# Kernel optimization log

Hardware: AMD Instinct MI355X
Metric: run time of the kernel (lower is better)

The kernel has to match this reference:

```python
import jax, jax.numpy as jnp
import numpy as np

B, T = 32, 64            # batch, max caption length
E = 14                   # encoded image grid
ENC_D, DEC_D, ATT_D = 2048, 512, 512
PATCH, CH = 32, 3
FLAT = PATCH * PATCH * CH   # 3072
EMB = 256
PAD = PATCH // 2 + PATCH // 4  # 24
IMG = 512


def setup_inputs() -> dict:
    key = jax.random.key(0)
    ks = jax.random.split(key, 20)
    w = lambda k, shp: (0.02 * jax.random.normal(k, shp)).astype(jnp.float32)
    z = lambda *shp: jnp.zeros(shp, jnp.float32)
    lengths = jnp.concatenate(
        [jnp.array([[T]], jnp.int32),
         jax.random.randint(ks[4], (B - 1, 1), 1, T + 1, dtype=jnp.int32)], axis=0)
    return dict(
        encoder_out=jax.random.normal(ks[0], (B, E, E, ENC_D), jnp.float32),
        imgs=jax.random.normal(ks[1], (B, CH, IMG, IMG), jnp.float32),
        sequence=jax.random.randint(ks[2], (B, T, 2), 0, IMG - PATCH, dtype=jnp.int32),
        sequence_offset=jax.random.normal(ks[3], (B, T, 2), jnp.float32),
        caption_lengths=lengths,
        W_pe=w(ks[5], (EMB, FLAT)), b_pe=z(EMB),
        W_enc_att=w(ks[6], (ATT_D, ENC_D)), b_enc_att=z(ATT_D),
        W_dec_att=w(ks[7], (ATT_D, DEC_D)), b_dec_att=z(ATT_D),
        w_full=w(ks[8], (ATT_D,)), b_full=jnp.zeros((), jnp.float32),
        W_init_h=w(ks[9], (DEC_D, ENC_D + EMB)), b_init_h=z(DEC_D),
        W_init_c=w(ks[10], (DEC_D, ENC_D + EMB)), b_init_c=z(DEC_D),
        W_fb=w(ks[11], (ENC_D, DEC_D)), b_fb=z(ENC_D),
        W_ih=w(ks[12], (4 * DEC_D, ENC_D + EMB)), b_ih=z(4 * DEC_D),
        W_hh=w(ks[13], (4 * DEC_D, DEC_D)), b_hh=z(4 * DEC_D),
        W_fc=w(ks[14], (2, DEC_D)), b_fc=z(2),
        W_stop=w(ks[15], (1, DEC_D)), b_stop=z(1),
    )


def _extract_patches(imgs, seq):
    # imgs: [B,C,H,W] int keypoints seq: [B,T,2] (x,y); deterministic shift=0
    padded = jnp.pad(imgs, ((0, 0), (0, 0), (PAD, PAD), (PAD, PAD)))
    def one(img, kp):
        return jax.lax.dynamic_slice(img, (0, kp[1], kp[0]), (CH, PATCH, PATCH))
    return jax.vmap(lambda img, kps: jax.vmap(lambda kp: one(img, kp))(kps))(padded, seq)


def reference(encoder_out, imgs, sequence, sequence_offset, caption_lengths,
              W_pe, b_pe, W_enc_att, b_enc_att, W_dec_att, b_dec_att, w_full, b_full,
              W_init_h, b_init_h, W_init_c, b_init_c, W_fb, b_fb,
              W_ih, b_ih, W_hh, b_hh, W_fc, b_fc, W_stop, b_stop):
    lengths = caption_lengths[:, 0]
    sort_ind = jnp.argsort(-lengths)            # descending, like torch sort
    lengths = lengths[sort_ind]
    enc = encoder_out[sort_ind].reshape(B, -1, ENC_D)   # [B,P,ENC_D]
    imgs_s = imgs[sort_ind]
    seq_s = sequence[sort_ind]
    seq_off_s = sequence_offset[sort_ind]

    # patch embedding (dropout is identity in eval mode)
    patches = _extract_patches(imgs_s, seq_s).reshape(B, T, FLAT)
    emb = patches @ W_pe.T + b_pe               # [B,T,EMB]

    # init hidden state
    init_in = jnp.concatenate([enc.mean(axis=1), emb[:, 0, :]], axis=1)
    h = init_in @ W_init_h.T + b_init_h
    c = init_in @ W_init_c.T + b_init_c

    att1 = enc @ W_enc_att.T + b_enc_att        # [B,P,A] (loop-invariant)

    def step(carry, xs):
        h, c = carry
        emb_t, t = xs
        att2 = h @ W_dec_att.T + b_dec_att                       # [B,A]
        scores = jnp.einsum('bpa,a->bp', jax.nn.relu(att1 + att2[:, None, :]), w_full) + b_full
        alpha = jax.nn.softmax(scores, axis=1)                   # [B,P]
        awe = jnp.einsum('bpd,bp->bd', enc, alpha)               # [B,ENC_D]
        gate = jax.nn.sigmoid(h @ W_fb.T + b_fb)
        x = jnp.concatenate([gate * awe, emb_t], axis=1)
        gates = x @ W_ih.T + b_ih + h @ W_hh.T + b_hh
        i, f, g, o = jnp.split(gates, 4, axis=1)
        c_new = jax.nn.sigmoid(f) * c + jax.nn.sigmoid(i) * jnp.tanh(g)
        h_new = jax.nn.sigmoid(o) * jnp.tanh(c_new)
        mask = (t < lengths)[:, None]
        preds = jnp.where(mask, h_new @ W_fc.T + b_fc, 0.0)
        preds_stop = jnp.where(mask, jax.nn.sigmoid(h_new @ W_stop.T + b_stop), 0.0)
        alpha_m = jnp.where(mask, alpha, 0.0)
        h = jnp.where(mask, h_new, h)
        c = jnp.where(mask, c_new, c)
        return (h, c), (preds, preds_stop, alpha_m)

    (_, _), (P, PS, AL) = jax.lax.scan(step, (h, c), (emb.transpose(1, 0, 2), jnp.arange(T)))
    predictions = P.transpose(1, 0, 2)          # [B,T,2]
    predictions_stop = PS.transpose(1, 0, 2)    # [B,T,1]
    alphas = AL.transpose(1, 0, 2)              # [B,T,P]
    return predictions, predictions_stop, seq_off_s, lengths, alphas, sort_ind
```

## Files before the change

kernel.cpp:

```cpp
#include <hip/hip_runtime.h>

#define Bn 32
#define Tn 64
#define Pn 196
#define ENCD 2048
#define DECD 512
#define XDIM 2304

typedef unsigned short u16;
typedef __attribute__((ext_vector_type(8))) short bf16x8;
typedef __attribute__((ext_vector_type(4))) float f32x4;

#define MF(a,b,c) __builtin_amdgcn_mfma_f32_16x16x32_bf16(a,b,c,0,0,0)

static __device__ __forceinline__ u16 f2bf(float f){
  unsigned int u = __float_as_uint(f);
  unsigned int r = u + 0x7FFFu + ((u >> 16) & 1u);
  return (u16)(r >> 16);
}
static __device__ __forceinline__ float bf2f(u16 u){
  return __uint_as_float(((unsigned int)u) << 16);
}

#define O_PRED   0
#define O_STOP   4096
#define O_SEQOFF 6144
#define O_LEN    10240
#define O_ALPHA  10272
#define O_SORT   411680

#define WS_SORT    0
#define WS_LEN     32
#define WS_C       64
#define WS_PA      16448
#define WS_SCP     163904
#define WS_ENCM    215104
#define WS_EMB0    280640
#define WS_BCOMB   288832
#define US_H0      800000
#define US_H1      816384
#define US_XA      832768
#define US_EMBBF   898304
#define US_ATT1T   1422592
#define US_ENC     4830464
#define US_WAP     17675520
#define US_WIHE    20067584
#define US_WIH2    20591872
#define US_GEMB    24786176
#define US_PATCH   20591872
#define US_WPEB    26883328
#define US_WEA     27931904

__global__ void k_prep(const int* __restrict__ caplen, int* __restrict__ ws_sort,
                       int* __restrict__ ws_len, float* __restrict__ out){
  __shared__ int len[32];
  int i = threadIdx.x;
  if (i < 32) len[i] = caplen[i];
  __syncthreads();
  if (i < 32){
    int li = len[i], r = 0;
    for (int j = 0; j < 32; j++){
      int lj = len[j];
      r += (lj > li) || (lj == li && j < i);
    }
    ws_sort[r] = i;
    ws_len[r]  = li;
    out[O_LEN + r]  = (float)li;
    out[O_SORT + r] = (float)i;
  }
}

__global__ __launch_bounds__(256) void k_stageA(const float* __restrict__ enc,
    const float* __restrict__ imgs, const int* __restrict__ seq,
    const float* __restrict__ W_pe, const float* __restrict__ Wea,
    const float* __restrict__ seqoff, const int* __restrict__ srt,
    u16* __restrict__ encbf, float* __restrict__ encm, u16* __restrict__ patches,
    u16* __restrict__ wpeb, u16* __restrict__ wead, float* __restrict__ out){
  int blk = blockIdx.x, tid = threadIdx.x;
  if (blk < 6272){
    int m = blk;
    int b = m / 196, p = m - b*196;
    const float* src = enc + ((size_t)srt[b]*196 + p)*ENCD;
    u16* d = encbf + (size_t)m*ENCD;
    int i = tid*8;
    float4 v0 = *(const float4*)(src + i);
    float4 v1 = *(const float4*)(src + i + 4);
    bf16x8 s;
    s[0]=(short)f2bf(v0.x); s[1]=(short)f2bf(v0.y); s[2]=(short)f2bf(v0.z); s[3]=(short)f2bf(v0.w);
    s[4]=(short)f2bf(v1.x); s[5]=(short)f2bf(v1.y); s[6]=(short)f2bf(v1.z); s[7]=(short)f2bf(v1.w);
    *(bf16x8*)(d + i) = s;
  } else if (blk < 6528){
    int r = blk - 6272;
    int b = r >> 3, dc = r & 7;
    int d = dc*256 + tid;
    const float* ep = enc + ((size_t)srt[b]*196)*ENCD + d;
    float s = 0.f;
    #pragma unroll 4
    for (int p = 0; p < Pn; p++) s += ep[(size_t)p*ENCD];
    encm[b*ENCD + d] = s * (1.f/196.f);
  } else if (blk < 8576){
    int r = blk - 6528;
    int b = r>>6, t = r&63;
    int sb = srt[b];
    int x0 = seq[(sb*64+t)*2 + 0], y0 = seq[(sb*64+t)*2 + 1];
    const float* img = imgs + (size_t)sb*3*512*512;
    u16* dst = patches + (size_t)(b*64+t)*3072;
    for (int idx = tid; idx < 3072; idx += 256){
      int c = idx>>10, rem = idx&1023, i = rem>>5, j = rem&31;
      int yy = y0 + i - 24, xx = x0 + j - 24;
      float v = 0.f;
      if ((unsigned)yy < 512u && (unsigned)xx < 512u) v = img[((size_t)c*512 + yy)*512 + xx];
      dst[idx] = f2bf(v);
    }
  } else if (blk < 9344){
    int i = ((blk - 8576)*256 + tid)*4;
    float4 v = *(const float4*)(W_pe + i);
    wpeb[i+0] = f2bf(v.x); wpeb[i+1] = f2bf(v.y);
    wpeb[i+2] = f2bf(v.z); wpeb[i+3] = f2bf(v.w);
  } else if (blk < 9856){
    int r = blk - 9344;
    for (int i = tid; i < 2048; i += 256)
      wead[(size_t)r*2048 + i] = f2bf(Wea[(size_t)r*2048 + i]);
  } else {
    int idx = (blk - 9856)*256 + tid;
    int b = idx >> 7, r = idx & 127;
    out[O_SEQOFF + idx] = seqoff[srt[b]*128 + r];
  }
}

__global__ __launch_bounds__(256) void k_stageB(const u16* __restrict__ patches,
    const u16* __restrict__ wpeb, const float* __restrict__ b_pe,
    const u16* __restrict__ encbf, const u16* __restrict__ wead,
    const float* __restrict__ bea,
    u16* __restrict__ embbf, float* __restrict__ emb0, u16* __restrict__ att1T){
  __shared__ u16 A[64*138];
  int blk = blockIdx.x, tid = threadIdx.x;
  int wv = tid>>6, lane = tid&63, lr = lane&15, lh = lane>>4;
  if (blk < 128){
    int mb = blk >> 2, nb = blk & 3;
    int m0 = mb*64;
    f32x4 acc[4];
    #pragma unroll
    for (int mt = 0; mt < 4; mt++) acc[mt] = (f32x4){0,0,0,0};
    for (int kc = 0; kc < 24; kc++){
      __syncthreads();
      {
        int row = tid>>2, seg = tid&3;
        const u16* src = patches + (size_t)(m0 + row)*3072 + kc*128 + seg*32;
        #pragma unroll
        for (int i = 0; i < 4; i++)
          *(bf16x8*)&A[row*138 + seg*32 + i*8] = *(const bf16x8*)(src + i*8);
      }
      __syncthreads();
      #pragma unroll
      for (int ki = 0; ki < 4; ki++){
        bf16x8 bv = *(const bf16x8*)&wpeb[(size_t)(nb*64 + wv*16 + lr)*3072 + kc*128 + ki*32 + lh*8];
        #pragma unroll
        for (int mt = 0; mt < 4; mt++){
          bf16x8 av = *(const bf16x8*)&A[(mt*16 + lr)*138 + ki*32 + lh*8];
          acc[mt] = MF(av, bv, acc[mt]);
        }
      }
    }
    int n = nb*64 + wv*16 + lr;
    float bias = b_pe[n];
    #pragma unroll
    for (int mt = 0; mt < 4; mt++){
      #pragma unroll
      for (int r = 0; r < 4; r++){
        int t = mt*16 + lh*4 + r;
        float val = acc[mt][r] + bias;
        embbf[(size_t)(m0 + t)*256 + n] = f2bf(val);
        if (t == 0) emb0[mb*256 + n] = val;
      }
    }
  } else {
    int ab = blk - 128;
    int mb = ab >> 2, nb = ab & 3;
    int m0 = mb*64;
    f32x4 acc[4][2];
    #pragma unroll
    for (int mt = 0; mt < 4; mt++){ acc[mt][0] = (f32x4){0,0,0,0}; acc[mt][1] = (f32x4){0,0,0,0}; }
    for (int kc = 0; kc < 16; kc++){
      __syncthreads();
      {
        int row = tid>>2, seg = tid&3;
        const u16* src = encbf + (size_t)(m0 + row)*2048 + kc*128 + seg*32;
        #pragma unroll
        for (int i = 0; i < 4; i++)
          *(bf16x8*)&A[row*138 + seg*32 + i*8] = *(const bf16x8*)(src + i*8);
      }
      __syncthreads();
      #pragma unroll
      for (int ki = 0; ki < 4; ki++){
        bf16x8 av[4];
        #pragma unroll
        for (int mt = 0; mt < 4; mt++)
          av[mt] = *(const bf16x8*)&A[(mt*16 + lr)*138 + ki*32 + lh*8];
        #pragma unroll
        for (int nt = 0; nt < 2; nt++){
          const u16* wp = wead + (size_t)(nb*128 + wv*32 + nt*16 + lr)*2048 + kc*128 + ki*32 + lh*8;
          bf16x8 bv = *(const bf16x8*)wp;
          #pragma unroll
          for (int mt = 0; mt < 4; mt++) acc[mt][nt] = MF(av[mt], bv, acc[mt][nt]);
        }
      }
    }
    #pragma unroll
    for (int nt = 0; nt < 2; nt++){
      int n = nb*128 + wv*32 + nt*16 + lr;
      float bias = bea[n];
      #pragma unroll
      for (int mt = 0; mt < 4; mt++){
        #pragma unroll
        for (int r = 0; r < 4; r++){
          int m = m0 + mt*16 + lh*4 + r;
          int bb = m / 196, pp = m - bb*196;
          att1T[((size_t)bb*512 + n)*208 + pp] = f2bf(acc[mt][nt][r] + bias);
        }
      }
    }
  }
}

__global__ __launch_bounds__(256) void k_stageC(const float* __restrict__ Wih,
    const float* __restrict__ Whh, const float* __restrict__ Wdec,
    const float* __restrict__ Wfb, const float* __restrict__ Wfc,
    const float* __restrict__ Wstop, const float* __restrict__ bih,
    const float* __restrict__ bhh,
    const float* __restrict__ encm, const float* __restrict__ emb0,
    const float* __restrict__ Wh, const float* __restrict__ Wc,
    u16* __restrict__ WIH2, u16* __restrict__ WIHE, u16* __restrict__ WAP,
    float* __restrict__ bcomb, float* __restrict__ part){
  int blk = blockIdx.x, tid = threadIdx.x;
  if (blk < 2048){
    int r = blk, jp = (r & 511)*4 + (r >> 9);
    for (int i = tid; i < 2304; i += 256){
      u16 v = f2bf(Wih[(size_t)r*2304 + i]);
      if (i < 2048) WIH2[(size_t)jp*2048 + i] = v;
      else          WIHE[(size_t)jp*256 + (i - 2048)] = v;
    }
  } else if (blk < 6720){
    int j = blk - 2048;
    const float* src;
    if (j < 512)        src = Wdec + (size_t)j*512;
    else if (j < 2560)  src = Wfb + (size_t)(j-512)*512;
    else if (j < 4608)  src = Whh + (size_t)(j-2560)*512;
    else if (j == 4608) src = Wfc;
    else if (j == 4609) src = Wfc + 512;
    else if (j == 4610) src = Wstop;
    else src = 0;
    for (int i = tid; i < 512; i += 256)
      WAP[(size_t)j*512 + i] = src ? f2bf(src[i]) : (u16)0;
  } else if (blk < 6728){
    int jp = (blk - 6720)*256 + tid;
    int r = (jp & 3)*512 + (jp >> 2);
    bcomb[jp] = bih[r] + bhh[r];
  } else {
    int ib = blk - 6728;
    int kc = ib >> 4, jb = ib & 15;
    int wv = tid>>6, lane = tid&63, lr = lane&15, lh = lane>>4;
    int j = jb*64 + wv*16 + lr;
    const float* wbase = (j < 512) ? (Wh + (size_t)j*XDIM) : (Wc + (size_t)(j-512)*XDIM);
    f32x4 acc0 = {0,0,0,0}, acc1 = {0,0,0,0};
    #pragma unroll 2
    for (int kk = 0; kk < 576; kk += 32){
      int k = kc*576 + kk + lh*8;
      float4 w0 = *(const float4*)(wbase + k);
      float4 w1 = *(const float4*)(wbase + k + 4);
      bf16x8 bv;
      bv[0]=(short)f2bf(w0.x); bv[1]=(short)f2bf(w0.y); bv[2]=(short)f2bf(w0.z); bv[3]=(short)f2bf(w0.w);
      bv[4]=(short)f2bf(w1.x); bv[5]=(short)f2bf(w1.y); bv[6]=(short)f2bf(w1.z); bv[7]=(short)f2bf(w1.w);
      float4 x0, x1, y0, y1;
      if (k < 2048){
        x0 = *(const float4*)(encm + (size_t)lr*2048 + k);
        x1 = *(const float4*)(encm + (size_t)lr*2048 + k + 4);
        y0 = *(const float4*)(encm + (size_t)(16+lr)*2048 + k);
        y1 = *(const float4*)(encm + (size_t)(16+lr)*2048 + k + 4);
      } else {
        int ke = k - 2048;
        x0 = *(const float4*)(emb0 + (size_t)lr*256 + ke);
        x1 = *(const float4*)(emb0 + (size_t)lr*256 + ke + 4);
        y0 = *(const float4*)(emb0 + (size_t)(16+lr)*256 + ke);
        y1 = *(const float4*)(emb0 + (size_t)(16+lr)*256 + ke + 4);
      }
      bf16x8 a0, a1;
      a0[0]=(short)f2bf(x0.x); a0[1]=(short)f2bf(x0.y); a0[2]=(short)f2bf(x0.z); a0[3]=(short)f2bf(x0.w);
      a0[4]=(short)f2bf(x1.x); a0[5]=(short)f2bf(x1.y); a0[6]=(short)f2bf(x1.z); a0[7]=(short)f2bf(x1.w);
      a1[0]=(short)f2bf(y0.x); a1[1]=(short)f2bf(y0.y); a1[2]=(short)f2bf(y0.z); a1[3]=(short)f2bf(y0.w);
      a1[4]=(short)f2bf(y1.x); a1[5]=(short)f2bf(y1.y); a1[6]=(short)f2bf(y1.z); a1[7]=(short)f2bf(y1.w);
      acc0 = MF(a0, bv, acc0);
      acc1 = MF(a1, bv, acc1);
    }
    #pragma unroll
    for (int r = 0; r < 4; ++r){
      int b0 = lh*4 + r, b1 = 16 + b0;
      part[(size_t)(kc*32 + b0)*1024 + j] = acc0[r];
      part[(size_t)(kc*32 + b1)*1024 + j] = acc1[r];
    }
  }
}

__global__ __launch_bounds__(256) void k_stageD(const u16* __restrict__ embbf,
    const u16* __restrict__ WIHE, const float* __restrict__ part,
    const float* __restrict__ bh, const float* __restrict__ bc,
    u16* __restrict__ gemb, u16* __restrict__ h_bf, float* __restrict__ c){
  __shared__ u16 A[64*266];
  int blk = blockIdx.x, tid = threadIdx.x;
  if (blk < 256){
    int m0 = (blk >> 3)*64, n0 = (blk & 7)*256;
    int wv = tid>>6, lane = tid&63, lr = lane&15, lh = lane>>4;
    {
      int row = tid>>2, seg = tid&3;
      const u16* src = embbf + (size_t)(m0 + row)*256 + seg*64;
      #pragma unroll
      for (int i = 0; i < 8; i++)
        *(bf16x8*)&A[row*266 + seg*64 + i*8] = *(const bf16x8*)(src + i*8);
    }
    __syncthreads();
    f32x4 acc[4][4];
    #pragma unroll
    for (int mt = 0; mt < 4; mt++)
      #pragma unroll
      for (int nt = 0; nt < 4; nt++) acc[mt][nt] = (f32x4){0,0,0,0};
    #pragma unroll
    for (int ki = 0; ki < 8; ki++){
      bf16x8 av[4];
      #pragma unroll
      for (int mt = 0; mt < 4; mt++)
        av[mt] = *(const bf16x8*)&A[(mt*16 + lr)*266 + ki*32 + lh*8];
      #pragma unroll
      for (int nt = 0; nt < 4; nt++){
        bf16x8 bv = *(const bf16x8*)&WIHE[(size_t)(n0 + wv*64 + nt*16 + lr)*256 + ki*32 + lh*8];
        #pragma unroll
        for (int mt = 0; mt < 4; mt++) acc[mt][nt] = MF(av[mt], bv, acc[mt][nt]);
      }
    }
    #pragma unroll
    for (int nt = 0; nt < 4; nt++){
      int n = n0 + wv*64 + nt*16 + lr;
      #pragma unroll
      for (int mt = 0; mt < 4; mt++)
        #pragma unroll
        for (int r = 0; r < 4; r++)
          gemb[(size_t)(m0 + mt*16 + lh*4 + r)*2048 + n] = f2bf(acc[mt][nt][r]);
    }
  } else {
    int idx = (blk - 256)*256 + tid;
    int b = idx >> 10, j = idx & 1023;
    float s = part[(size_t)b*1024 + j] + part[(size_t)(32+b)*1024 + j]
            + part[(size_t)(64+b)*1024 + j] + part[(size_t)(96+b)*1024 + j];
    if (j < 512) h_bf[(size_t)b*512 + j] = f2bf(s + bh[j]);
    else         c[(size_t)b*512 + (j-512)] = s + bc[j-512];
  }
}

__global__ __launch_bounds__(256) void kAB(const u16* __restrict__ h, const u16* __restrict__ WAP,
    float* __restrict__ pA, const u16* __restrict__ att1T,
    const float* __restrict__ bdec, const float* __restrict__ wfull,
    float* __restrict__ scp, const float* __restrict__ bfc, const float* __restrict__ bstop,
    const int* __restrict__ len, float* __restrict__ out, int t){
  int blk = blockIdx.x, tid = threadIdx.x;
  if (t == 64 && blk != 64) return;
  if (blk < 65){
    __shared__ u16 HL[32*522];
    int wv = tid>>6, lane = tid&63, lr = lane&15, lh = lane>>4;
    for (int i = tid; i < 4096; i += 256){
      unsigned long long v = ((const unsigned long long*)h)[i];
      int row = i >> 7, col = (i & 127)*4;
      *(unsigned long long*)&HL[row*522 + col] = v;
    }
    __syncthreads();
    int j0 = 512 + blk*64 + wv*16;
    f32x4 acc0 = {0,0,0,0}, acc1 = {0,0,0,0};
    #pragma unroll 4
    for (int ki = 0; ki < 16; ++ki){
      bf16x8 bv = *(const bf16x8*)&WAP[(size_t)(j0+lr)*512 + ki*32 + lh*8];
      bf16x8 a0 = *(const bf16x8*)&HL[lr*522 + ki*32 + lh*8];
      bf16x8 a1 = *(const bf16x8*)&HL[(16+lr)*522 + ki*32 + lh*8];
      acc0 = MF(a0, bv, acc0);
      acc1 = MF(a1, bv, acc1);
    }
    int j = j0 + lr;
    if (j < 4608){
      #pragma unroll
      for (int r = 0; r < 4; ++r){
        pA[(size_t)(lh*4+r)*4608 + j]    = acc0[r];
        pA[(size_t)(lh*4+r+16)*4608 + j] = acc1[r];
      }
    } else if (j < 4611 && t > 0){
      int jj = j - 4608, tm1 = t - 1;
      #pragma unroll
      for (int r = 0; r < 4; ++r){
        #pragma unroll
        for (int hb = 0; hb < 2; ++hb){
          int b0 = lh*4 + r + hb*16;
          float val = hb ? acc1[r] : acc0[r];
          bool mk = tm1 < len[b0];
          if (jj < 2) out[O_PRED + ((size_t)b0*64 + tm1)*2 + jj] = mk ? val + bfc[jj] : 0.f;
          else        out[O_STOP + (size_t)b0*64 + tm1] =
                        mk ? 1.f/(1.f + expf(-(val + bstop[0]))) : 0.f;
        }
      }
    }
  } else {
    int kb = blk - 65, b = kb >> 3, ac = kb & 7;
    if (t >= len[b]) return;
    __shared__ u16 hL[512];
    __shared__ float a2s[64], wfs[64];
    if (tid < 128)
      ((unsigned long long*)hL)[tid] = ((const unsigned long long*)(h + (size_t)b*512))[tid];
    if (tid < 64) wfs[tid] = wfull[ac*64 + tid];
    __syncthreads();
    {
      int a = tid >> 2, q = tid & 3;
      const u16* wrow = WAP + (size_t)(ac*64 + a)*512 + q*128;
      const u16* hrow = hL + q*128;
      float acc = 0.f;
      #pragma unroll
      for (int i = 0; i < 16; ++i){
        bf16x8 wv8 = *(const bf16x8*)(wrow + i*8);
        bf16x8 hv8 = *(const bf16x8*)(hrow + i*8);
        #pragma unroll
        for (int e = 0; e < 8; ++e) acc += bf2f((u16)hv8[e]) * bf2f((u16)wv8[e]);
      }
      acc += __shfl_xor(acc, 1);
      acc += __shfl_xor(acc, 2);
      if (q == 0) a2s[a] = acc + bdec[ac*64 + a];
    }
    __syncthreads();
    int p = tid;
    if (p < 196){
      const u16* col = att1T + ((size_t)b*512 + ac*64)*208 + p;
      float acc = 0.f;
      #pragma unroll 8
      for (int a = 0; a < 64; ++a)
        acc += fmaxf(bf2f(col[(size_t)a*208]) + a2s[a], 0.f) * wfs[a];
      scp[(size_t)(b*8 + ac)*200 + p] = acc;
    }
  }
}

__global__ __launch_bounds__(256) void kB2(const float* __restrict__ scp,
    const float* __restrict__ pA, const u16* __restrict__ encbf,
    const float* __restrict__ bfull, const float* __restrict__ bfb,
    u16* __restrict__ xa, const int* __restrict__ len, float* __restrict__ out, int t){
  int b = blockIdx.x >> 3, dc = blockIdx.x & 7;
  int tid = threadIdx.x, wv = tid>>6, lane = tid&63;
  if (t >= len[b]){
    if (dc == 0 && tid < 196) out[O_ALPHA + ((size_t)b*64 + t)*196 + tid] = 0.f;
    return;
  }
  __shared__ float ev[200], redf[4], bcx[2];
  float s = -1e30f;
  if (tid < 196){
    s = bfull[0];
    #pragma unroll
    for (int q = 0; q < 8; ++q) s += scp[(size_t)(b*8 + q)*200 + tid];
  }
  float m = s;
  #pragma unroll
  for (int o = 32; o; o >>= 1) m = fmaxf(m, __shfl_down(m, o));
  if (lane == 0) redf[wv] = m;
  __syncthreads();
  if (tid == 0) bcx[0] = fmaxf(fmaxf(redf[0],redf[1]), fmaxf(redf[2],redf[3]));
  __syncthreads();
  float e = (tid < 196) ? expf(s - bcx[0]) : 0.f;
  if (tid < 200) ev[tid] = (tid < 196) ? e : 0.f;
  float sm = e;
  #pragma unroll
  for (int o = 32; o; o >>= 1) sm += __shfl_down(sm, o);
  __syncthreads();
  if (lane == 0) redf[wv] = sm;
  __syncthreads();
  if (tid == 0) bcx[1] = redf[0]+redf[1]+redf[2]+redf[3];
  __syncthreads();
  float ssum = bcx[1];
  int d = dc*256 + tid;
  const u16* ep = encbf + (size_t)(b*196)*ENCD + d;
  float q[8];
  #pragma unroll
  for (int j = 0; j < 8; ++j) q[j] = 0.f;
  #pragma unroll 2
  for (int p = 0; p < 192; p += 8){
    #pragma unroll
    for (int j = 0; j < 8; ++j)
      q[j] += ev[p+j]*bf2f(ep[(size_t)(p+j)*ENCD]);
  }
  #pragma unroll
  for (int j = 0; j < 4; ++j)
    q[j] += ev[192+j]*bf2f(ep[(size_t)(192+j)*ENCD]);
  float awe = (((q[0]+q[1])+(q[2]+q[3])) + ((q[4]+q[5])+(q[6]+q[7]))) / ssum;
  float gp = pA[(size_t)b*4608 + 512 + d] + bfb[d];
  float gate = 1.f/(1.f + expf(-gp));
  xa[(size_t)b*2048 + d] = f2bf(gate * awe);
  if (dc == 0 && tid < 196) out[O_ALPHA + ((size_t)b*64 + t)*196 + tid] = ev[tid]/ssum;
}

__global__ __launch_bounds__(512) void kC(const u16* __restrict__ xa,
    const u16* __restrict__ hc, u16* __restrict__ hn, float* __restrict__ c,
    const u16* __restrict__ WIH2, const float* __restrict__ pA,
    const float* __restrict__ bcomb, const u16* __restrict__ gemb,
    const int* __restrict__ len, int t){
  int tid = threadIdx.x, wv = tid>>6, lane = tid&63, lr = lane&15, lh = lane>>4;
  int jp0 = blockIdx.x*16;
  __shared__ float red[8*512];
  f32x4 acc0 = {0,0,0,0}, acc1 = {0,0,0,0};
  #pragma unroll
  for (int ks = 0; ks < 8; ++ks){
    int k = wv*256 + ks*32;
    bf16x8 a0 = *(const bf16x8*)&xa[(size_t)lr*2048 + k + lh*8];
    bf16x8 a1 = *(const bf16x8*)&xa[(size_t)(16+lr)*2048 + k + lh*8];
    bf16x8 bv = *(const bf16x8*)&WIH2[(size_t)(jp0+lr)*2048 + k + lh*8];
    acc0 = MF(a0, bv, acc0);
    acc1 = MF(a1, bv, acc1);
  }
  #pragma unroll
  for (int r = 0; r < 4; ++r){
    red[wv*512 + ((lh*4+r) << 4) + lr]    = acc0[r];
    red[wv*512 + ((16+lh*4+r) << 4) + lr] = acc1[r];
  }
  __syncthreads();
  {
    int b = tid >> 4, jl = tid & 15, e = jl & 3;
    int jp = jp0 + jl, u = jp >> 2;
    float g = 0.f;
    #pragma unroll
    for (int w = 0; w < 8; ++w) g += red[w*512 + tid];
    g += bcomb[jp] + bf2f(gemb[((size_t)b*64 + t)*2048 + jp])
       + pA[(size_t)b*4608 + 2560 + e*512 + u];
    float sv = (e == 2) ? tanhf(g) : 1.f/(1.f + expf(-g));
    float vb = __shfl_xor(sv, 1), vc = __shfl_xor(sv, 2), vd = __shfl_xor(vb, 2);
    float i_s = (e==0)?sv:(e==1)?vb:(e==2)?vc:vd;
    float f_s = (e==1)?sv:(e==0)?vb:(e==3)?vc:vd;
    float g_t = (e==2)?sv:(e==3)?vb:(e==0)?vc:vd;
    float o_s = (e==3)?sv:(e==2)?vb:(e==1)?vc:vd;
    float cold = c[(size_t)b*512 + u];
    float hold = bf2f(hc[(size_t)b*512 + u]);
    bool mk = t < len[b];
    float cn = mk ? (f_s*cold + i_s*g_t) : cold;
    float hv = mk ? (o_s * tanhf(cn)) : hold;
    if (e == 0){
      c[(size_t)b*512 + u] = cn;
      hn[(size_t)b*512 + u] = f2bf(hv);
    }
  }
}

extern "C" void kernel_launch(void* const* d_in, const int* in_sizes, int n_in,
                              void* d_out, int out_size, void* d_ws, size_t ws_size,
                              hipStream_t stream){
  (void)in_sizes; (void)n_in; (void)out_size; (void)ws_size;
  const float* enc_out   = (const float*)d_in[0];
  const float* imgs      = (const float*)d_in[1];
  const int*   seq       = (const int*)d_in[2];
  const float* seqoff    = (const float*)d_in[3];
  const int*   caplen    = (const int*)d_in[4];
  const float* W_pe      = (const float*)d_in[5];
  const float* b_pe      = (const float*)d_in[6];
  const float* W_enc_att = (const float*)d_in[7];
  const float* b_enc_att = (const float*)d_in[8];
  const float* W_dec_att = (const float*)d_in[9];
  const float* b_dec_att = (const float*)d_in[10];
  const float* w_full    = (const float*)d_in[11];
  const float* b_full    = (const float*)d_in[12];
  const float* W_init_h  = (const float*)d_in[13];
  const float* b_init_h  = (const float*)d_in[14];
  const float* W_init_c  = (const float*)d_in[15];
  const float* b_init_c  = (const float*)d_in[16];
  const float* W_fb      = (const float*)d_in[17];
  const float* b_fb      = (const float*)d_in[18];
  const float* W_ih      = (const float*)d_in[19];
  const float* b_ih      = (const float*)d_in[20];
  const float* W_hh      = (const float*)d_in[21];
  const float* b_hh      = (const float*)d_in[22];
  const float* W_fc      = (const float*)d_in[23];
  const float* b_fc      = (const float*)d_in[24];
  const float* W_stop    = (const float*)d_in[25];
  const float* b_stop    = (const float*)d_in[26];

  float* out = (float*)d_out;
  float* ws  = (float*)d_ws;
  int*   wsi = (int*)d_ws;
  u16*   us  = (u16*)d_ws;

  u16* H[2] = { us + US_H0, us + US_H1 };

  k_prep<<<1, 64, 0, stream>>>(caplen, wsi + WS_SORT, wsi + WS_LEN, out);
  k_stageA<<<9872, 256, 0, stream>>>(enc_out, imgs, seq, W_pe, W_enc_att, seqoff,
                                     wsi + WS_SORT,
                                     us + US_ENC, ws + WS_ENCM, us + US_PATCH,
                                     us + US_WPEB, us + US_WEA, out);
  k_stageB<<<520, 256, 0, stream>>>(us + US_PATCH, us + US_WPEB, b_pe,
                                    us + US_ENC, us + US_WEA, b_enc_att,
                                    us + US_EMBBF, ws + WS_EMB0, us + US_ATT1T);
  k_stageC<<<6792, 256, 0, stream>>>(W_ih, W_hh, W_dec_att, W_fb, W_fc, W_stop,
                                     b_ih, b_hh,
                                     ws + WS_ENCM, ws + WS_EMB0, W_init_h, W_init_c,
                                     us + US_WIH2, us + US_WIHE, us + US_WAP,
                                     ws + WS_BCOMB, ws + WS_PA);
  k_stageD<<<384, 256, 0, stream>>>(us + US_EMBBF, us + US_WIHE, ws + WS_PA,
                                    b_init_h, b_init_c,
                                    us + US_GEMB, H[0], ws + WS_C);

  for (int t = 0; t < Tn; ++t){
    kAB<<<321, 256, 0, stream>>>(H[t & 1], us + US_WAP, ws + WS_PA, us + US_ATT1T,
                                 b_dec_att, w_full, ws + WS_SCP, b_fc, b_stop,
                                 wsi + WS_LEN, out, t);
    kB2<<<256, 256, 0, stream>>>(ws + WS_SCP, ws + WS_PA, us + US_ENC, b_full, b_fb,
                                 us + US_XA, wsi + WS_LEN, out, t);
    kC<<<128, 512, 0, stream>>>(us + US_XA, H[t & 1], H[(t + 1) & 1], ws + WS_C,
                                us + US_WIH2, ws + WS_PA, ws + WS_BCOMB, us + US_GEMB,
                                wsi + WS_LEN, t);
  }
  kAB<<<65, 256, 0, stream>>>(H[0], us + US_WAP, ws + WS_PA, us + US_ATT1T,
                              b_dec_att, w_full, ws + WS_SCP, b_fc, b_stop,
                              wsi + WS_LEN, out, 64);
}
```

Measured before the change: 1.835 ms.

## Fuse per-timestep decoder kernels into one persistent cooperative kernel with grid barriers

Replaces the 193 per-timestep launches (kAB, kB2, kC for each of 64 steps) with a single cooperative persistent kernel of 256 workgroups. The steps are separated by atomic-counter grid barriers, and shared data goes through agent-scope relaxed atomic loads and stores. The aim is to remove kernel launch overhead and inter-kernel gaps on the serial recurrence. It also keeps the LSTM cell state in registers, splits the attention-score reduction into 4 chunks instead of 8, and moves the prediction/stop head into a dedicated block. The risks are barrier spin cost, relaxed-ordering correctness, and fewer blocks doing work in each phase.

```diff
diff --git a/kernel.cpp b/kernel.cpp
--- a/kernel.cpp
+++ b/kernel.cpp
@@ -6,6 +6,7 @@
 #define ENCD 2048
 #define DECD 512
 #define XDIM 2304
+#define NWG 256
 
 typedef unsigned short u16;
 typedef __attribute__((ext_vector_type(8))) short bf16x8;
@@ -20,6 +21,39 @@
 }
 static __device__ __forceinline__ float bf2f(u16 u){
   return __uint_as_float(((unsigned int)u) << 16);
+}
+
+static __device__ __forceinline__ void cstore_u32(unsigned* p, unsigned v){
+  __hip_atomic_store(p, v, __ATOMIC_RELAXED, __HIP_MEMORY_SCOPE_AGENT);
+}
+static __device__ __forceinline__ unsigned cload_u32(const unsigned* p){
+  return __hip_atomic_load((unsigned*)p, __ATOMIC_RELAXED, __HIP_MEMORY_SCOPE_AGENT);
+}
+static __device__ __forceinline__ void cstore_f32(float* p, float v){
+  cstore_u32((unsigned*)p, __float_as_uint(v));
+}
+static __device__ __forceinline__ float cload_f32(const float* p){
+  return __uint_as_float(cload_u32((const unsigned*)p));
+}
+static __device__ __forceinline__ unsigned long long cload_u64(const unsigned long long* p){
+  return __hip_atomic_load((unsigned long long*)p, __ATOMIC_RELAXED, __HIP_MEMORY_SCOPE_AGENT);
+}
+static __device__ __forceinline__ bf16x8 cload_bf8(const u16* p){
+  union { unsigned long long q[2]; bf16x8 v; } u;
+  u.q[0] = cload_u64((const unsigned long long*)p);
+  u.q[1] = cload_u64((const unsigned long long*)(p + 4));
+  return u.v;
+}
+
+static __device__ __forceinline__ void gbar(unsigned* cnt, unsigned target){
+  __syncthreads();
+  if (threadIdx.x == 0){
+    __hip_atomic_fetch_add(cnt, 1u, __ATOMIC_RELAXED, __HIP_MEMORY_SCOPE_AGENT);
+    while (__hip_atomic_load(cnt, __ATOMIC_RELAXED, __HIP_MEMORY_SCOPE_AGENT) < target)
+      __builtin_amdgcn_s_sleep(1);
+  }
+  asm volatile("" ::: "memory");
+  __syncthreads();
 }
 
 #define O_PRED   0
@@ -37,6 +71,7 @@
 #define WS_ENCM    215104
 #define WS_EMB0    280640
 #define WS_BCOMB   288832
+#define WS_BAR     290880
 #define US_H0      800000
 #define US_H1      816384
 #define US_XA      832768
@@ -52,9 +87,11 @@
 #define US_WEA     27931904
 
 __global__ void k_prep(const int* __restrict__ caplen, int* __restrict__ ws_sort,
-                       int* __restrict__ ws_len, float* __restrict__ out){
+                       int* __restrict__ ws_len, unsigned* __restrict__ bar,
+                       float* __restrict__ out){
   __shared__ int len[32];
   int i = threadIdx.x;
+  if (i == 0) *bar = 0u;
   if (i < 32) len[i] = caplen[i];
   __syncthreads();
   if (i < 32){
@@ -355,195 +392,221 @@
   }
 }
 
-__global__ __launch_bounds__(256) void kAB(const u16* __restrict__ h, const u16* __restrict__ WAP,
-    float* __restrict__ pA, const u16* __restrict__ att1T,
-    const float* __restrict__ bdec, const float* __restrict__ wfull,
-    float* __restrict__ scp, const float* __restrict__ bfc, const float* __restrict__ bstop,
-    const int* __restrict__ len, float* __restrict__ out, int t){
-  int blk = blockIdx.x, tid = threadIdx.x;
-  if (t == 64 && blk != 64) return;
-  if (blk < 65){
-    __shared__ u16 HL[32*522];
-    int wv = tid>>6, lane = tid&63, lr = lane&15, lh = lane>>4;
-    for (int i = tid; i < 4096; i += 256){
-      unsigned long long v = ((const unsigned long long*)h)[i];
-      int row = i >> 7, col = (i & 127)*4;
-      *(unsigned long long*)&HL[row*522 + col] = v;
-    }
-    __syncthreads();
-    int j0 = 512 + blk*64 + wv*16;
-    f32x4 acc0 = {0,0,0,0}, acc1 = {0,0,0,0};
-    #pragma unroll 4
-    for (int ki = 0; ki < 16; ++ki){
-      bf16x8 bv = *(const bf16x8*)&WAP[(size_t)(j0+lr)*512 + ki*32 + lh*8];
-      bf16x8 a0 = *(const bf16x8*)&HL[lr*522 + ki*32 + lh*8];
-      bf16x8 a1 = *(const bf16x8*)&HL[(16+lr)*522 + ki*32 + lh*8];
-      acc0 = MF(a0, bv, acc0);
-      acc1 = MF(a1, bv, acc1);
-    }
-    int j = j0 + lr;
-    if (j < 4608){
+struct LoopP {
+  unsigned* bar;
+  float* pA; float* scp; const float* c0; const float* bcomb;
+  u16* h0; u16* h1; u16* xa;
+  const u16* att1T; const u16* enc; const u16* gemb;
+  const u16* WAP; const u16* WIH2;
+  const float* bdec; const float* wfull; const float* bfull; const float* bfb;
+  const float* bfc; const float* bstop;
+  const int* len; float* out;
+};
+
+__global__ __launch_bounds__(256) void k_loop(LoopP P){
+  const int blk = blockIdx.x, tid = threadIdx.x;
+  const int wv = tid>>6, lane = tid&63, lr = lane&15, lh = lane>>4;
+  __shared__ __align__(16) char SM[33536];
+  unsigned bt = 0;
+  float creg0 = 0.f, creg1 = 0.f;
+
+  for (int t = 0; t <= 64; ++t){
+    const u16* hc = (t & 1) ? P.h1 : P.h0;
+    if (blk < 64 && t < 64){
+      u16* HL = (u16*)SM;
+      for (int i = tid; i < 4096; i += 256){
+        unsigned long long v = cload_u64(((const unsigned long long*)hc) + i);
+        int row = i >> 7, col = (i & 127)*4;
+        *(unsigned long long*)&HL[row*522 + col] = v;
+      }
+      __syncthreads();
+      int j0 = 512 + blk*64 + wv*16;
+      f32x4 acc0 = {0,0,0,0}, acc1 = {0,0,0,0};
+      #pragma unroll 4
+      for (int ki = 0; ki < 16; ++ki){
+        bf16x8 bv = *(const bf16x8*)&P.WAP[(size_t)(j0+lr)*512 + ki*32 + lh*8];
+        bf16x8 a0 = *(const bf16x8*)&HL[lr*522 + ki*32 + lh*8];
+        bf16x8 a1 = *(const bf16x8*)&HL[(16+lr)*522 + ki*32 + lh*8];
+        acc0 = MF(a0, bv, acc0);
+        acc1 = MF(a1, bv, acc1);
+      }
+      int j = j0 + lr;
       #pragma unroll
       for (int r = 0; r < 4; ++r){
-        pA[(size_t)(lh*4+r)*4608 + j]    = acc0[r];
-        pA[(size_t)(lh*4+r+16)*4608 + j] = acc1[r];
-      }
-    } else if (j < 4611 && t > 0){
-      int jj = j - 4608, tm1 = t - 1;
+        cstore_f32(&P.pA[(size_t)(lh*4+r)*4608 + j], acc0[r]);
+        cstore_f32(&P.pA[(size_t)(lh*4+r+16)*4608 + j], acc1[r]);
+      }
+    } else if (blk == 64 && t > 0){
+      if (tid < 192){
+        int task = tid >> 1, q = tid & 1;
+        int b = task / 3, rw = task - b*3;
+        const u16* hrow = hc + (size_t)b*512 + q*256;
+        const u16* wrow = P.WAP + (size_t)(4608 + rw)*512 + q*256;
+        float acc = 0.f;
+        #pragma unroll 4
+        for (int i = 0; i < 32; ++i){
+          bf16x8 hv8 = cload_bf8(hrow + i*8);
+          bf16x8 wv8 = *(const bf16x8*)(wrow + i*8);
+          #pragma unroll
+          for (int e = 0; e < 8; ++e) acc += bf2f((u16)hv8[e]) * bf2f((u16)wv8[e]);
+        }
+        acc += __shfl_xor(acc, 1);
+        if (q == 0){
+          int tm1 = t - 1;
+          bool mk = tm1 < P.len[b];
+          if (rw < 2) P.out[O_PRED + ((size_t)b*64 + tm1)*2 + rw] = mk ? acc + P.bfc[rw] : 0.f;
+          else        P.out[O_STOP + (size_t)b*64 + tm1] =
+                        mk ? 1.f/(1.f + expf(-(acc + P.bstop[0]))) : 0.f;
+        }
+      }
+    } else if (blk > 64 && blk < 193 && t < 64){
+      int kb = blk - 65, b = kb >> 2, ch = kb & 3;
+      if (t < P.len[b]){
+        u16* hL = (u16*)SM;
+        float* a2s = (float*)(SM + 1024);
+        float* wfs = a2s + 128;
+        if (tid < 128)
+          ((unsigned long long*)hL)[tid] = cload_u64(((const unsigned long long*)(hc + (size_t)b*512)) + tid);
+        if (tid < 128) wfs[tid] = P.wfull[ch*128 + tid];
+        __syncthreads();
+        {
+          int a = tid >> 1, q = tid & 1;
+          const u16* wrow = P.WAP + (size_t)(ch*128 + a)*512 + q*256;
+          const u16* hrow = hL + q*256;
+          float acc = 0.f;
+          #pragma unroll 4
+          for (int i = 0; i < 32; ++i){
+            bf16x8 wv8 = *(const bf16x8*)(wrow + i*8);
+            bf16x8 hv8 = *(const bf16x8*)(hrow + i*8);
+            #pragma unroll
+            for (int e = 0; e < 8; ++e) acc += bf2f((u16)hv8[e]) * bf2f((u16)wv8[e]);
+          }
+          acc += __shfl_xor(acc, 1);
+          if (q == 0) a2s[a] = acc + P.bdec[ch*128 + a];
+        }
+        __syncthreads();
+        int p = tid;
+        if (p < 196){
+          const u16* col = P.att1T + ((size_t)b*512 + ch*128)*208 + p;
+          float acc = 0.f;
+          #pragma unroll 8
+          for (int a = 0; a < 128; ++a)
+            acc += fmaxf(bf2f(col[(size_t)a*208]) + a2s[a], 0.f) * wfs[a];
+          cstore_f32(&P.scp[(size_t)(b*4 + ch)*200 + p], acc);
+        }
+      }
+    }
+    if (t == 64) break;
+    bt += NWG; gbar(P.bar, bt);
+
+    {
+      int b = blk >> 3, dc = blk & 7;
+      if (t < P.len[b]){
+        float* ev   = (float*)SM;
+        float* redf = ev + 200;
+        float* bcx  = redf + 4;
+        float s = -1e30f;
+        if (tid < 196){
+          s = P.bfull[0];
+          #pragma unroll
+          for (int q = 0; q < 4; ++q) s += cload_f32(&P.scp[(size_t)(b*4 + q)*200 + tid]);
+        }
+        float m = s;
+        #pragma unroll
+        for (int o = 32; o; o >>= 1) m = fmaxf(m, __shfl_down(m, o));
+        if (lane == 0) redf[wv] = m;
+        __syncthreads();
+        if (tid == 0) bcx[0] = fmaxf(fmaxf(redf[0],redf[1]), fmaxf(redf[2],redf[3]));
+        __syncthreads();
+        float e = (tid < 196) ? expf(s - bcx[0]) : 0.f;
+        if (tid < 200) ev[tid] = (tid < 196) ? e : 0.f;
+        float sm = e;
+        #pragma unroll
+        for (int o = 32; o; o >>= 1) sm += __shfl_down(sm, o);
+        __syncthreads();
+        if (lane == 0) redf[wv] = sm;
+        __syncthreads();
+        if (tid == 0) bcx[1] = redf[0]+redf[1]+redf[2]+redf[3];
+        __syncthreads();
+        float ssum = bcx[1];
+        int d = dc*256 + tid;
+        const u16* ep = P.enc + (size_t)(b*196)*ENCD + d;
+        float q[8];
+        #pragma unroll
+        for (int j = 0; j < 8; ++j) q[j] = 0.f;
+        #pragma unroll 2
+        for (int p = 0; p < 192; p += 8){
+          #pragma unroll
+          for (int j = 0; j < 8; ++j)
+            q[j] += ev[p+j]*bf2f(ep[(size_t)(p+j)*ENCD]);
+        }
+        #pragma unroll
+        for (int j = 0; j < 4; ++j)
+          q[j] += ev[192+j]*bf2f(ep[(size_t)(192+j)*ENCD]);
+        float awe = (((q[0]+q[1])+(q[2]+q[3])) + ((q[4]+q[5])+(q[6]+q[7]))) / ssum;
+        float gp = cload_f32(&P.pA[(size_t)b*4608 + 512 + d]) + P.bfb[d];
+        float gate = 1.f/(1.f + expf(-gp));
+        unsigned hb16 = f2bf(gate * awe);
+        unsigned po = (unsigned)__shfl_xor((int)hb16, 1);
+        if ((tid & 1) == 0)
+          cstore_u32(((unsigned*)P.xa) + (size_t)b*1024 + (d >> 1), hb16 | (po << 16));
+        if (dc == 0 && tid < 196) P.out[O_ALPHA + ((size_t)b*64 + t)*196 + tid] = ev[tid]/ssum;
+      } else {
+        if (dc == 0 && tid < 196) P.out[O_ALPHA + ((size_t)b*64 + t)*196 + tid] = 0.f;
+      }
+    }
+    bt += NWG; gbar(P.bar, bt);
+
+    if (blk < 128){
+      u16* hn = (t & 1) ? P.h0 : P.h1;
+      float* red = (float*)SM;
+      int jp0 = blk*16;
+      f32x4 acc0 = {0,0,0,0}, acc1 = {0,0,0,0};
+      #pragma unroll 4
+      for (int ks = 0; ks < 16; ++ks){
+        int k = wv*512 + ks*32;
+        bf16x8 a0 = cload_bf8(&P.xa[(size_t)lr*2048 + k + lh*8]);
+        bf16x8 a1 = cload_bf8(&P.xa[(size_t)(16+lr)*2048 + k + lh*8]);
+        bf16x8 bv = *(const bf16x8*)&P.WIH2[(size_t)(jp0+lr)*2048 + k + lh*8];
+        acc0 = MF(a0, bv, acc0);
+        acc1 = MF(a1, bv, acc1);
+      }
+      __syncthreads();
       #pragma unroll
       for (int r = 0; r < 4; ++r){
-        #pragma unroll
-        for (int hb = 0; hb < 2; ++hb){
-          int b0 = lh*4 + r + hb*16;
-          float val = hb ? acc1[r] : acc0[r];
-          bool mk = tm1 < len[b0];
-          if (jj < 2) out[O_PRED + ((size_t)b0*64 + tm1)*2 + jj] = mk ? val + bfc[jj] : 0.f;
-          else        out[O_STOP + (size_t)b0*64 + tm1] =
-                        mk ? 1.f/(1.f + expf(-(val + bstop[0]))) : 0.f;
-        }
-      }
-    }
-  } else {
-    int kb = blk - 65, b = kb >> 3, ac = kb & 7;
-    if (t >= len[b]) return;
-    __shared__ u16 hL[512];
-    __shared__ float a2s[64], wfs[64];
-    if (tid < 128)
-      ((unsigned long long*)hL)[tid] = ((const unsigned long long*)(h + (size_t)b*512))[tid];
-    if (tid < 64) wfs[tid] = wfull[ac*64 + tid];
-    __syncthreads();
-    {
-      int a = tid >> 2, q = tid & 3;
-      const u16* wrow = WAP + (size_t)(ac*64 + a)*512 + q*128;
-      const u16* hrow = hL + q*128;
-      float acc = 0.f;
-      #pragma unroll
-      for (int i = 0; i < 16; ++i){
-        bf16x8 wv8 = *(const bf16x8*)(wrow + i*8);
-        bf16x8 hv8 = *(const bf16x8*)(hrow + i*8);
-        #pragma unroll
-        for (int e = 0; e < 8; ++e) acc += bf2f((u16)hv8[e]) * bf2f((u16)wv8[e]);
-      }
-      acc += __shfl_xor(acc, 1);
-      acc += __shfl_xor(acc, 2);
-      if (q == 0) a2s[a] = acc + bdec[ac*64 + a];
-    }
-    __syncthreads();
-    int p = tid;
-    if (p < 196){
-      const u16* col = att1T + ((size_t)b*512 + ac*64)*208 + p;
-      float acc = 0.f;
-      #pragma unroll 8
-      for (int a = 0; a < 64; ++a)
-        acc += fmaxf(bf2f(col[(size_t)a*208]) + a2s[a], 0.f) * wfs[a];
-      scp[(size_t)(b*8 + ac)*200 + p] = acc;
-    }
-  }
-}
-
-__global__ __launch_bounds__(256) void kB2(const float* __restrict__ scp,
-    const float* __restrict__ pA, const u16* __restrict__ encbf,
-    const float* __restrict__ bfull, const float* __restrict__ bfb,
-    u16* __restrict__ xa, const int* __restrict__ len, float* __restrict__ out, int t){
-  int b = blockIdx.x >> 3, dc = blockIdx.x & 7;
-  int tid = threadIdx.x, wv = tid>>6, lane = tid&63;
-  if (t >= len[b]){
-    if (dc == 0 && tid < 196) out[O_ALPHA + ((size_t)b*64 + t)*196 + tid] = 0.f;
-    return;
-  }
-  __shared__ float ev[200], redf[4], bcx[2];
-  float s = -1e30f;
-  if (tid < 196){
-    s = bfull[0];
-    #pragma unroll
-    for (int q = 0; q < 8; ++q) s += scp[(size_t)(b*8 + q)*200 + tid];
-  }
-  float m = s;
-  #pragma unroll
-  for (int o = 32; o; o >>= 1) m = fmaxf(m, __shfl_down(m, o));
-  if (lane == 0) redf[wv] = m;
-  __syncthreads();
-  if (tid == 0) bcx[0] = fmaxf(fmaxf(redf[0],redf[1]), fmaxf(redf[2],redf[3]));
-  __syncthreads();
-  float e = (tid < 196) ? expf(s - bcx[0]) : 0.f;
-  if (tid < 200) ev[tid] = (tid < 196) ? e : 0.f;
-  float sm = e;
-  #pragma unroll
-  for (int o = 32; o; o >>= 1) sm += __shfl_down(sm, o);
-  __syncthreads();
-  if (lane == 0) redf[wv] = sm;
-  __syncthreads();
-  if (tid == 0) bcx[1] = redf[0]+redf[1]+redf[2]+redf[3];
-  __syncthreads();
-  float ssum = bcx[1];
-  int d = dc*256 + tid;
-  const u16* ep = encbf + (size_t)(b*196)*ENCD + d;
-  float q[8];
-  #pragma unroll
-  for (int j = 0; j < 8; ++j) q[j] = 0.f;
-  #pragma unroll 2
-  for (int p = 0; p < 192; p += 8){
-    #pragma unroll
-    for (int j = 0; j < 8; ++j)
-      q[j] += ev[p+j]*bf2f(ep[(size_t)(p+j)*ENCD]);
-  }
-  #pragma unroll
-  for (int j = 0; j < 4; ++j)
-    q[j] += ev[192+j]*bf2f(ep[(size_t)(192+j)*ENCD]);
-  float awe = (((q[0]+q[1])+(q[2]+q[3])) + ((q[4]+q[5])+(q[6]+q[7]))) / ssum;
-  float gp = pA[(size_t)b*4608 + 512 + d] + bfb[d];
-  float gate = 1.f/(1.f + expf(-gp));
-  xa[(size_t)b*2048 + d] = f2bf(gate * awe);
-  if (dc == 0 && tid < 196) out[O_ALPHA + ((size_t)b*64 + t)*196 + tid] = ev[tid]/ssum;
-}
-
-__global__ __launch_bounds__(512) void kC(const u16* __restrict__ xa,
-    const u16* __restrict__ hc, u16* __restrict__ hn, float* __restrict__ c,
-    const u16* __restrict__ WIH2, const float* __restrict__ pA,
-    const float* __restrict__ bcomb, const u16* __restrict__ gemb,
-    const int* __restrict__ len, int t){
-  int tid = threadIdx.x, wv = tid>>6, lane = tid&63, lr = lane&15, lh = lane>>4;
-  int jp0 = blockIdx.x*16;
-  __shared__ float red[8*512];
-  f32x4 acc0 = {0,0,0,0}, acc1 = {0,0,0,0};
-  #pragma unroll
-  for (int ks = 0; ks < 8; ++ks){
-    int k = wv*256 + ks*32;
-    bf16x8 a0 = *(const bf16x8*)&xa[(size_t)lr*2048 + k + lh*8];
-    bf16x8 a1 = *(const bf16x8*)&xa[(size_t)(16+lr)*2048 + k + lh*8];
-    bf16x8 bv = *(const bf16x8*)&WIH2[(size_t)(jp0+lr)*2048 + k + lh*8];
-    acc0 = MF(a0, bv, acc0);
-    acc1 = MF(a1, bv, acc1);
-  }
-  #pragma unroll
-  for (int r = 0; r < 4; ++r){
-    red[wv*512 + ((lh*4+r) << 4) + lr]    = acc0[r];
-    red[wv*512 + ((16+lh*4+r) << 4) + lr] = acc1[r];
-  }
-  __syncthreads();
-  {
-    int b = tid >> 4, jl = tid & 15, e = jl & 3;
-    int jp = jp0 + jl, u = jp >> 2;
-    float g = 0.f;
-    #pragma unroll
-    for (int w = 0; w < 8; ++w) g += red[w*512 + tid];
-    g += bcomb[jp] + bf2f(gemb[((size_t)b*64 + t)*2048 + jp])
-       + pA[(size_t)b*4608 + 2560 + e*512 + u];
-    float sv = (e == 2) ? tanhf(g) : 1.f/(1.f + expf(-g));
-    float vb = __shfl_xor(sv, 1), vc = __shfl_xor(sv, 2), vd = __shfl_xor(vb, 2);
-    float i_s = (e==0)?sv:(e==1)?vb:(e==2)?vc:vd;
-    float f_s = (e==1)?sv:(e==0)?vb:(e==3)?vc:vd;
-    float g_t = (e==2)?sv:(e==3)?vb:(e==0)?vc:vd;
-    float o_s = (e==3)?sv:(e==2)?vb:(e==1)?vc:vd;
-    float cold = c[(size_t)b*512 + u];
-    float hold = bf2f(hc[(size_t)b*512 + u]);
-    bool mk = t < len[b];
-    float cn = mk ? (f_s*cold + i_s*g_t) : cold;
-    float hv = mk ? (o_s * tanhf(cn)) : hold;
-    if (e == 0){
-      c[(size_t)b*512 + u] = cn;
-      hn[(size_t)b*512 + u] = f2bf(hv);
-    }
+        red[wv*512 + ((lh*4+r) << 4) + lr]    = acc0[r];
+        red[wv*512 + ((16+lh*4+r) << 4) + lr] = acc1[r];
+      }
+      __syncthreads();
+      #pragma unroll
+      for (int pass = 0; pass < 2; ++pass){
+        int idx = pass*256 + tid;
+        int b = idx >> 4, jl = idx & 15, e = jl & 3;
+        int jp = jp0 + jl, u = jp >> 2;
+        float g = red[idx] + red[512+idx] + red[1024+idx] + red[1536+idx];
+        g += P.bcomb[jp] + bf2f(P.gemb[((size_t)b*64 + t)*2048 + jp])
+           + cload_f32(&P.pA[(size_t)b*4608 + 2560 + e*512 + u]);
+        float creg = pass ? creg1 : creg0;
+        if (t == 0) creg = P.c0[(size_t)b*512 + u];
+        float sv = (e == 2) ? tanhf(g) : 1.f/(1.f + expf(-g));
+        float vb = __shfl_xor(sv, 1), vc = __shfl_xor(sv, 2), vd = __shfl_xor(vb, 2);
+        float i_s = (e==0)?sv:(e==1)?vb:(e==2)?vc:vd;
+        float f_s = (e==1)?sv:(e==0)?vb:(e==3)?vc:vd;
+        float g_t = (e==2)?sv:(e==3)?vb:(e==0)?vc:vd;
+        float o_s = (e==3)?sv:(e==2)?vb:(e==1)?vc:vd;
+        unsigned hp = cload_u32((const unsigned*)(hc + (size_t)b*512 + (u & ~1)));
+        float hold = bf2f((u16)((u & 1) ? (hp >> 16) : (hp & 0xFFFF)));
+        bool mk = t < P.len[b];
+        float cn = mk ? (f_s*creg + i_s*g_t) : creg;
+        float hv = mk ? (o_s * tanhf(cn)) : hold;
+        if (pass) creg1 = cn; else creg0 = cn;
+        unsigned hb = (unsigned)f2bf(hv);
+        unsigned pu = (unsigned)__shfl_xor((int)hb, 4);
+        if ((idx & 7) == 0)
+          cstore_u32((unsigned*)(hn + (size_t)b*512 + u), hb | (pu << 16));
+      }
+    }
+    bt += NWG; gbar(P.bar, bt);
   }
 }
 
@@ -584,9 +647,8 @@
   int*   wsi = (int*)d_ws;
   u16*   us  = (u16*)d_ws;
 
-  u16* H[2] = { us + US_H0, us + US_H1 };
-
-  k_prep<<<1, 64, 0, stream>>>(caplen, wsi + WS_SORT, wsi + WS_LEN, out);
+  k_prep<<<1, 64, 0, stream>>>(caplen, wsi + WS_SORT, wsi + WS_LEN,
+                               (unsigned*)(ws + WS_BAR), out);
   k_stageA<<<9872, 256, 0, stream>>>(enc_out, imgs, seq, W_pe, W_enc_att, seqoff,
                                      wsi + WS_SORT,
                                      us + US_ENC, ws + WS_ENCM, us + US_PATCH,
@@ -601,19 +663,17 @@
                                      ws + WS_BCOMB, ws + WS_PA);
   k_stageD<<<384, 256, 0, stream>>>(us + US_EMBBF, us + US_WIHE, ws + WS_PA,
                                     b_init_h, b_init_c,
-                                    us + US_GEMB, H[0], ws + WS_C);
-
-  for (int t = 0; t < Tn; ++t){
-    kAB<<<321, 256, 0, stream>>>(H[t & 1], us + US_WAP, ws + WS_PA, us + US_ATT1T,
-                                 b_dec_att, w_full, ws + WS_SCP, b_fc, b_stop,
-                                 wsi + WS_LEN, out, t);
-    kB2<<<256, 256, 0, stream>>>(ws + WS_SCP, ws + WS_PA, us + US_ENC, b_full, b_fb,
-                                 us + US_XA, wsi + WS_LEN, out, t);
-    kC<<<128, 512, 0, stream>>>(us + US_XA, H[t & 1], H[(t + 1) & 1], ws + WS_C,
-                                us + US_WIH2, ws + WS_PA, ws + WS_BCOMB, us + US_GEMB,
-                                wsi + WS_LEN, t);
-  }
-  kAB<<<65, 256, 0, stream>>>(H[0], us + US_WAP, ws + WS_PA, us + US_ATT1T,
-                              b_dec_att, w_full, ws + WS_SCP, b_fc, b_stop,
-                              wsi + WS_LEN, out, 64);
-}
+                                    us + US_GEMB, us + US_H0, ws + WS_C);
+
+  LoopP P;
+  P.bar = (unsigned*)(ws + WS_BAR);
+  P.pA = ws + WS_PA; P.scp = ws + WS_SCP; P.c0 = ws + WS_C; P.bcomb = ws + WS_BCOMB;
+  P.h0 = us + US_H0; P.h1 = us + US_H1; P.xa = us + US_XA;
+  P.att1T = us + US_ATT1T; P.enc = us + US_ENC; P.gemb = us + US_GEMB;
+  P.WAP = us + US_WAP; P.WIH2 = us + US_WIH2;
+  P.bdec = b_dec_att; P.wfull = w_full; P.bfull = b_full; P.bfb = b_fb;
+  P.bfc = b_fc; P.bstop = b_stop;
+  P.len = wsi + WS_LEN; P.out = out;
+  void* ka[1] = { (void*)&P };
+  hipLaunchCooperativeKernel((const void*)k_loop, dim3(NWG), dim3(256), ka, 0, stream);
+}
```

Result: slower. 4.233 ms (+130.7%).
